# Kernel optimization log

Measured on AMD Instinct MI355X. Metric: run time of the kernel, lower is better.

## Reference

```python
import jax, jax.numpy as jnp
import numpy as np

# dims
N, E, H, ED, G = 50000, 1000000, 64, 16, 512
IN_C, OUT_C, L, T, OUT_N = 39, 128, 3, 2, 1
SLOPE = 0.01  # negative slope used by F.leaky_relu and GATConv(negative_slope=0.01)


def _seg_softmax(a, seg, n):
    # numerically-stable softmax over edges grouped by target segment
    m = jax.ops.segment_max(a, seg, num_segments=n)
    m = jnp.where(jnp.isfinite(m), m, 0.0)
    e = jnp.exp(a - m[seg])
    s = jax.ops.segment_sum(e, seg, num_segments=n)
    return e / (s[seg] + 1e-16)


def _gru(inp, h, wi, wh, bi, bh):
    # torch.nn.GRUCell: gates ordered (r, z, n)
    gi = inp @ wi.T + bi
    gh = h @ wh.T + bh
    ir, iz, i_n = jnp.split(gi, 3, axis=-1)
    hr, hz, h_n = jnp.split(gh, 3, axis=-1)
    r = jax.nn.sigmoid(ir + hr)
    z = jax.nn.sigmoid(iz + hz)
    n = jnp.tanh(i_n + r * h_n)
    return (1.0 - z) * n + z * h


def _forward(x, edge_attr,
             lin1_w, lin1_b,
             g_lin1_w, g_att_l, g_att_r, g_lin2_w, g_bias,
             gru0_wi, gru0_wh, gru0_bi, gru0_bh,
             conv_lin_w, conv_att_src, conv_att_dst, conv_bias,
             grul_wi, grul_wh, grul_bi, grul_bh,
             mol_lin_w, mol_att_src, mol_att_dst, mol_bias,
             mgru_wi, mgru_wh, mgru_bi, mgru_bh,
             lin2_w, lin2_b,
             src, dst, batch):
    x = jax.nn.leaky_relu(x @ lin1_w.T + lin1_b, SLOPE)  # [N,H]

    # ---- GATEConv ----
    xj, xi = x[src], x[dst]                               # [E,H]
    t = jax.nn.leaky_relu(jnp.concatenate([xj, edge_attr], -1) @ g_lin1_w.T, SLOPE)
    a = jax.nn.leaky_relu(t @ g_att_l + xi @ g_att_r, SLOPE)
    a = _seg_softmax(a, dst, N)
    h = jax.ops.segment_sum((xj @ g_lin2_w.T) * a[:, None], dst, num_segments=N) + g_bias
    h = jax.nn.elu(h)
    x = jax.nn.relu(_gru(h, x, gru0_wi, gru0_wh, gru0_bi, gru0_bh))

    # ---- GATConv atom layers ----
    for l in range(L - 1):
        hs = x @ conv_lin_w[l].T                          # [N,H]
        a = jax.nn.leaky_relu((hs @ conv_att_src[l])[src] + (hs @ conv_att_dst[l])[dst], SLOPE)
        a = _seg_softmax(a, dst, N)
        h = jax.ops.segment_sum(hs[src] * a[:, None], dst, num_segments=N) + conv_bias[l]
        h = jax.nn.elu(h)
        x = jax.nn.relu(_gru(h, x, grul_wi[l], grul_wh[l], grul_bi[l], grul_bh[l]))

    # ---- molecule-level attention readout ----
    out = jax.nn.relu(jax.ops.segment_sum(x, batch, num_segments=G))  # [G,H]
    for _ in range(T):
        hs = x @ mol_lin_w.T                              # [N,H]  (atoms = sources)
        hd = out @ mol_lin_w.T                            # [G,H]  (mols = targets)
        a = jax.nn.leaky_relu(hs @ mol_att_src + (hd @ mol_att_dst)[batch], SLOPE)
        a = _seg_softmax(a, batch, G)
        h = jax.ops.segment_sum(hs * a[:, None], batch, num_segments=G) + mol_bias
        h = jax.nn.elu(h)
        out = jax.nn.relu(_gru(h, out, mgru_wi, mgru_wh, mgru_bi, mgru_bh))

    out = out @ lin2_w.T + lin2_b                         # [G,OUT_C]
    return jnp.concatenate([out[None]] * OUT_N, axis=0)   # [OUT_N,G,OUT_C]


def setup_inputs() -> dict:
    key = jax.random.key(0)
    it = iter(jax.random.split(key, 48))

    def p(*shape):
        return jax.random.normal(next(it), shape, jnp.float32) * 0.1

    d = {}
    d["x"] = jax.random.normal(next(it), (N, IN_C), jnp.float32)
    d["edge_index"] = jax.random.randint(next(it), (2, E), 0, N, dtype=jnp.int32)
    d["edge_attr"] = jax.random.normal(next(it), (E, ED), jnp.float32)
    d["batch"] = jnp.sort(jax.random.randint(next(it), (N,), 0, G, dtype=jnp.int32))

    d["lin1_w"], d["lin1_b"] = p(H, IN_C), p(H)
    d["g_lin1_w"] = p(H, H + ED)
    d["g_att_l"], d["g_att_r"] = p(H), p(H)
    d["g_lin2_w"], d["g_bias"] = p(H, H), p(H)
    d["gru0_wi"], d["gru0_wh"] = p(3 * H, H), p(3 * H, H)
    d["gru0_bi"], d["gru0_bh"] = p(3 * H), p(3 * H)
    d["conv_lin_w"] = p(L - 1, H, H)
    d["conv_att_src"], d["conv_att_dst"] = p(L - 1, H), p(L - 1, H)
    d["conv_bias"] = p(L - 1, H)
    d["grul_wi"], d["grul_wh"] = p(L - 1, 3 * H, H), p(L - 1, 3 * H, H)
    d["grul_bi"], d["grul_bh"] = p(L - 1, 3 * H), p(L - 1, 3 * H)
    d["mol_lin_w"] = p(H, H)
    d["mol_att_src"], d["mol_att_dst"] = p(H), p(H)
    d["mol_bias"] = p(H)
    d["mgru_wi"], d["mgru_wh"] = p(3 * H, H), p(3 * H, H)
    d["mgru_bi"], d["mgru_bh"] = p(3 * H), p(3 * H)
    d["lin2_w"], d["lin2_b"] = p(OUT_C, H), p(OUT_C)
    return d


def reference(x, edge_index, edge_attr, batch,
              lin1_w, lin1_b,
              g_lin1_w, g_att_l, g_att_r, g_lin2_w, g_bias,
              gru0_wi, gru0_wh, gru0_bi, gru0_bh,
              conv_lin_w, conv_att_src, conv_att_dst, conv_bias,
              grul_wi, grul_wh, grul_bi, grul_bh,
              mol_lin_w, mol_att_src, mol_att_dst, mol_bias,
              mgru_wi, mgru_wh, mgru_bi, mgru_bh,
              lin2_w, lin2_b):
    src, dst = edge_index[0], edge_index[1]
    return _forward(x, edge_attr,
                    lin1_w, lin1_b,
                    g_lin1_w, g_att_l, g_att_r, g_lin2_w, g_bias,
                    gru0_wi, gru0_wh, gru0_bi, gru0_bh,
                    conv_lin_w, conv_att_src, conv_att_dst, conv_bias,
                    grul_wi, grul_wh, grul_bi, grul_bh,
                    mol_lin_w, mol_att_src, mol_att_dst, mol_bias,
                    mgru_wi, mgru_wh, mgru_bi, mgru_bh,
                    lin2_w, lin2_b,
                    src, dst, batch)
```

## Files before the change

kernel.cpp:

```cpp
#include <hip/hip_runtime.h>
#include <math.h>

#define N_NODES 50000
#define N_EDGES 1000000
#define NGRAPH  512
#define INC     39
#define SB 200
#define SC 250
#define NBKT 196
#define BIN_BLK 4096

typedef __attribute__((ext_vector_type(8))) short bf16x8;
typedef __attribute__((ext_vector_type(4))) float f32x4;
typedef __attribute__((ext_vector_type(4))) int i32x4;

__device__ __forceinline__ float lrelu(float x){ return fmaxf(0.01f*x, x); }
__device__ __forceinline__ float fexp(float x){ return __builtin_amdgcn_exp2f(x*1.4426950408889634f); }
__device__ __forceinline__ float frcp(float x){ return __builtin_amdgcn_rcpf(x); }
__device__ __forceinline__ float eluf (float x){ return x > 0.f ? x : fexp(x) - 1.f; }
__device__ __forceinline__ float sigm (float x){ return frcp(1.f + fexp(-x)); }
__device__ __forceinline__ float ftanh(float x){
  x = fminf(fmaxf(x, -15.f), 15.f);
  float e = __builtin_amdgcn_exp2f(x*2.8853900817779268f);
  return (e - 1.f)*frcp(e + 1.f);
}
__device__ __forceinline__ float rdlane(float v, int l){
  return __int_as_float(__builtin_amdgcn_readlane(__float_as_int(v), l));
}
__device__ __forceinline__ unsigned pk_bf16(float a, float b){
  unsigned r;
  asm volatile("v_cvt_pk_bf16_f32 %0, %1, %2" : "=v"(r) : "v"(a), "v"(b));
  return r;
}
__device__ __forceinline__ float bl(unsigned p){ return __uint_as_float(p << 16); }
__device__ __forceinline__ float bh(unsigned p){ return __uint_as_float(p & 0xffff0000u); }

__global__ __launch_bounds__(256) void k_hist(const int* __restrict__ dst,
                                              int* __restrict__ cnt) {
  int e = blockIdx.x*256 + threadIdx.x;
  if (e < N_EDGES) atomicAdd(&cnt[dst[e]], 1);
}

__global__ __launch_bounds__(256) void k_scanA(const int* __restrict__ cnt,
                                               int* __restrict__ bsum) {
  __shared__ int s[256];
  int t = threadIdx.x, b = blockIdx.x;
  int v = (t < SC) ? cnt[b*SC + t] : 0;
  s[t] = v; __syncthreads();
  for (int off = 128; off > 0; off >>= 1) {
    if (t < off) s[t] += s[t+off];
    __syncthreads();
  }
  if (t == 0) bsum[b] = s[0];
}

__global__ __launch_bounds__(256) void k_scanB(const int* __restrict__ bsum,
                                               int* __restrict__ boff,
                                               int* __restrict__ rowptrN) {
  __shared__ int s[256];
  int t = threadIdx.x;
  int v = (t < SB) ? bsum[t] : 0;
  s[t] = v; __syncthreads();
  for (int off = 1; off < 256; off <<= 1) {
    int x = (t >= off) ? s[t-off] : 0;
    __syncthreads();
    s[t] += x;
    __syncthreads();
  }
  if (t < SB) boff[t] = s[t] - v;
  if (t == 0) rowptrN[0] = N_EDGES;
}

__global__ __launch_bounds__(256) void k_scanC(const int* __restrict__ cnt,
                                               const int* __restrict__ boff,
                                               int* __restrict__ rowptr) {
  __shared__ int s[256];
  int t = threadIdx.x, b = blockIdx.x;
  int idx = b*SC + t;
  int v = (t < SC) ? cnt[idx] : 0;
  s[t] = v; __syncthreads();
  for (int off = 1; off < 256; off <<= 1) {
    int x = (t >= off) ? s[t-off] : 0;
    __syncthreads();
    s[t] += x;
    __syncthreads();
  }
  if (t < SC) rowptr[idx] = boff[b] + s[t] - v;
}

__global__ __launch_bounds__(256) void k_bstart(const int* __restrict__ rowptr,
                                                int* __restrict__ bstart,
                                                int* __restrict__ bcur) {
  int b = threadIdx.x;
  if (b <= NBKT) {
    int idx = b*256; if (idx > N_NODES) idx = N_NODES;
    int v = rowptr[idx];
    bstart[b] = v;
    if (b < NBKT) bcur[b] = v;
  }
}

__global__ __launch_bounds__(1024) void k_binA(const int* __restrict__ dst,
                                               const int* __restrict__ src,
                                               const float* __restrict__ p,
                                               int* __restrict__ bcur,
                                               int2* __restrict__ binned) {
  __shared__ int lcnt[NBKT];
  __shared__ int lbase[NBKT];
  __shared__ int gbase[NBKT];
  __shared__ int tmp[256];
  __shared__ int totsh;
  __shared__ int2 stage[BIN_BLK];
  const int t = threadIdx.x;
  const int e0 = blockIdx.x * BIN_BLK;
  for (int i = t; i < NBKT; i += 1024) lcnt[i] = 0;
  __syncthreads();
  int myb[4], myr[4], myd[4], mys[4]; float myp[4];
  #pragma unroll
  for (int u = 0; u < 4; ++u) {
    int e = e0 + u*1024 + t;
    if (e < N_EDGES) {
      int d = dst[e];
      myd[u] = d; mys[u] = src[e]; myp[u] = p[e];
      int b = d >> 8;
      myb[u] = b;
      myr[u] = atomicAdd(&lcnt[b], 1);
    } else myb[u] = -1;
  }
  __syncthreads();
  if (t < 256) tmp[t] = (t < NBKT) ? lcnt[t] : 0;
  __syncthreads();
  for (int off = 1; off < 256; off <<= 1) {
    int v = (t >= off && t < 256) ? tmp[t-off] : 0;
    __syncthreads();
    if (t < 256) tmp[t] += v;
    __syncthreads();
  }
  if (t < NBKT) lbase[t] = tmp[t] - lcnt[t];
  if (t == NBKT-1) totsh = tmp[t];
  if (t < NBKT && lcnt[t] > 0) gbase[t] = atomicAdd(&bcur[t], lcnt[t]);
  __syncthreads();
  #pragma unroll
  for (int u = 0; u < 4; ++u) {
    if (myb[u] >= 0) {
      int x = (mys[u] & 0xffff) | ((myd[u] & 255) << 16) | (myb[u] << 24);
      stage[lbase[myb[u]] + myr[u]] = make_int2(x, __float_as_int(myp[u]));
    }
  }
  __syncthreads();
  const int tot = totsh;
  for (int i = t; i < tot; i += 1024) {
    int2 r = stage[i];
    int b = (unsigned)r.x >> 24;
    binned[gbase[b] + (i - lbase[b])] = r;
  }
}

__global__ __launch_bounds__(1024) void k_binB(const int* __restrict__ rowptr,
                                               const int* __restrict__ bstart,
                                               const int2* __restrict__ binned,
                                               int2* __restrict__ sorted) {
  __shared__ int lcnt[256];
  const int b = blockIdx.x;
  const int base = bstart[b], end = bstart[b+1];
  const int t = threadIdx.x;
  if (t < 256) lcnt[t] = 0;
  __syncthreads();
  for (int i = base + t; i < end; i += 1024) {
    int2 r = binned[i];
    int dlow = (r.x >> 16) & 255;
    int rank = atomicAdd(&lcnt[dlow], 1);
    int pos = rowptr[b*256 + dlow] + rank;
    sorted[pos] = r;
  }
}

__global__ __launch_bounds__(512) void k_gbound(const int* __restrict__ batch,
                                                int* __restrict__ gstart) {
  int g = threadIdx.x;
  int lo = 0, hi = N_NODES;
  while (lo < hi) { int mid = (lo+hi)>>1; if (batch[mid] < g) lo = mid+1; else hi = mid; }
  gstart[g] = lo;
  if (g == 0) gstart[NGRAPH] = N_NODES;
}

__global__ __launch_bounds__(256) void k_wpack(const float* __restrict__ wi,
                                               const float* __restrict__ wh,
                                               unsigned short* __restrict__ o) {
  int i = blockIdx.x*256 + threadIdx.x;
  if (i < 192*64)      o[i]          = (unsigned short)(pk_bf16(wi[i], 0.f) & 0xffffu);
  else if (i < 2*192*64) o[i]        = (unsigned short)(pk_bf16(wh[i - 192*64], 0.f) & 0xffffu);
}

__global__ __launch_bounds__(256) void k_lin1(const float* __restrict__ x,
                                              const float* __restrict__ W,
                                              const float* __restrict__ b,
                                              float* __restrict__ out,
                                              const float* __restrict__ v1,
                                              float* __restrict__ o1) {
  __shared__ float wl[64*41];
  for (int idx = threadIdx.x; idx < 64*INC; idx += 256) {
    int r = idx / INC, c = idx - r*INC;
    wl[r*41+c] = W[idx];
  }
  __syncthreads();
  const int lane = threadIdx.x & 63;
  const int base = blockIdx.x*32 + (threadIdx.x>>6)*8;
  float h[8];
  #pragma unroll
  for (int i = 0; i < 8; ++i) {
    int n = base + i;
    h[i] = (n < N_NODES && lane < INC) ? x[n*INC + lane] : 0.f;
  }
  float acc[8] = {0,0,0,0,0,0,0,0};
  #pragma unroll
  for (int k = 0; k < INC; ++k) {
    float wv = wl[lane*41+k];
    #pragma unroll
    for (int i = 0; i < 8; ++i) acc[i] += rdlane(h[i], k) * wv;
  }
  float bb = b[lane];
  float attv = v1[lane];
  #pragma unroll
  for (int i = 0; i < 8; ++i) {
    int n = base + i;
    if (n >= N_NODES) continue;
    float val = lrelu(acc[i] + bb);
    out[n*64+lane] = val;
    float p = val * attv;
    #pragma unroll
    for (int s2 = 32; s2 > 0; s2 >>= 1) p += __shfl_xor(p, s2, 64);
    if (lane == 0) o1[n] = p;
  }
}

__global__ __launch_bounds__(256) void k_mmdual(const float* __restrict__ in,
                                                const float* __restrict__ W1,
                                                const float* __restrict__ W2,
                                                unsigned short* __restrict__ ubf,
                                                unsigned* __restrict__ ypk, int R) {
  __shared__ float wl[128*65];
  for (int idx = threadIdx.x; idx < 4096; idx += 256) {
    int r = idx >> 6, c = idx & 63;
    wl[r*65+c]      = W1[r*80 + c];
    wl[(64+r)*65+c] = W2[r*64 + c];
  }
  __syncthreads();
  const int lane = threadIdx.x & 63;
  const int base = blockIdx.x*32 + (threadIdx.x>>6)*8;
  float h[8];
  #pragma unroll
  for (int i = 0; i < 8; ++i) { int n = base+i; h[i] = (n < R) ? in[n*64+lane] : 0.f; }
  float accU[8] = {0,0,0,0,0,0,0,0};
  float accY[8] = {0,0,0,0,0,0,0,0};
  for (int k = 0; k < 64; ++k) {
    float wu = wl[lane*65+k], wy = wl[(64+lane)*65+k];
    #pragma unroll
    for (int i = 0; i < 8; ++i) {
      float hk = rdlane(h[i], k);
      accU[i] += hk*wu; accY[i] += hk*wy;
    }
  }
  #pragma unroll
  for (int i = 0; i < 8; ++i) {
    int n = base+i; if (n >= R) continue;
    ubf[n*64 + lane] = (unsigned short)(pk_bf16(accU[i], 0.f) & 0xffffu);
    float partner = __shfl_xor(accY[i], 1, 64);
    if (!(lane & 1)) ypk[n*32 + (lane>>1)] = pk_bf16(accY[i], partner);
  }
}

__global__ __launch_bounds__(256) void k_mm64(const float* __restrict__ in,
                                              const float* __restrict__ W, int rs,
                                              float* __restrict__ out,
                                              unsigned* __restrict__ outp, int R,
                                              const float* __restrict__ v1,
                                              const float* __restrict__ v2,
                                              float* __restrict__ o1,
                                              float* __restrict__ o2) {
  __shared__ float wl[64*65];
  for (int idx = threadIdx.x; idx < 4096; idx += 256) {
    int r = idx >> 6, c = idx & 63;
    wl[r*65+c] = W[r*rs + c];
  }
  __syncthreads();
  const int lane = threadIdx.x & 63;
  const int base = blockIdx.x*32 + (threadIdx.x>>6)*8;
  float h[8];
  #pragma unroll
  for (int i = 0; i < 8; ++i) { int n = base+i; h[i] = (n < R) ? in[n*64+lane] : 0.f; }
  float acc[8] = {0,0,0,0,0,0,0,0};
  for (int k = 0; k < 64; ++k) {
    float wv = wl[lane*65+k];
    #pragma unroll
    for (int i = 0; i < 8; ++i) acc[i] += rdlane(h[i], k) * wv;
  }
  float v1v = v1 ? v1[lane] : 0.f;
  float v2v = v2 ? v2[lane] : 0.f;
  #pragma unroll
  for (int i = 0; i < 8; ++i) {
    int n = base+i; if (n >= R) continue;
    if (out) out[n*64+lane] = acc[i];
    if (outp) {
      float partner = __shfl_xor(acc[i], 1, 64);
      if ((lane & 1) == 0) outp[n*32 + (lane>>1)] = pk_bf16(acc[i], partner);
    }
    if (o1) {
      float p1 = acc[i]*v1v;
      float p2 = acc[i]*v2v;
      #pragma unroll
      for (int s2 = 32; s2 > 0; s2 >>= 1) { p1 += __shfl_xor(p1, s2, 64); p2 += __shfl_xor(p2, s2, 64); }
      if (lane == 0) { o1[n] = p1; if (o2) o2[n] = p2; }
    }
  }
}

__global__ __launch_bounds__(256) void k_escore(const int* __restrict__ srcarr,
                                                const float* __restrict__ ea,
                                                const float* __restrict__ glin1,
                                                const float* __restrict__ attl,
                                                const unsigned short* __restrict__ ubf,
                                                float* __restrict__ pout) {
  const int lane = threadIdx.x & 63;
  const int l15 = lane & 15, lg = lane >> 4;
  const int gw = blockIdx.x*4 + (threadIdx.x >> 6);
  if (gw >= N_EDGES/64) return;
  float attlv[4];
  unsigned Bu[4][2];
  #pragma unroll
  for (int c = 0; c < 4; ++c) {
    const float4 b = *(const float4*)&glin1[(c*16 + l15)*80 + 64 + lg*4];
    Bu[c][0] = pk_bf16(b.x, b.y);
    Bu[c][1] = pk_bf16(b.z, b.w);
    attlv[c] = attl[c*16 + l15];
  }
  const int i0 = gw*64;
  i32x4 sv[4];
  #pragma unroll
  for (int it = 0; it < 4; ++it)
    sv[it] = *(const i32x4*)&srcarr[i0 + it*16 + 4*lg];
  f32x4 a[4];
  #pragma unroll
  for (int it = 0; it < 4; ++it)
    a[it] = __builtin_nontemporal_load((const f32x4*)&ea[(size_t)(i0 + it*16 + l15)*16 + lg*4]);
  unsigned short ug0[4][4], ug1[4][4];
  #pragma unroll
  for (int c = 0; c < 4; ++c)
    #pragma unroll
    for (int r = 0; r < 4; ++r)
      ug0[c][r] = ubf[(size_t)sv[0][r]*64 + c*16 + l15];
  #pragma unroll
  for (int it = 0; it < 4; ++it) {
    if (it + 1 < 4) {
      #pragma unroll
      for (int c = 0; c < 4; ++c)
        #pragma unroll
        for (int r = 0; r < 4; ++r)
          ug1[c][r] = ubf[(size_t)sv[it+1][r]*64 + c*16 + l15];
    }
    union { bf16x8 v; unsigned u[4]; } A;
    A.u[0] = pk_bf16(a[it][0], a[it][1]);
    A.u[1] = pk_bf16(a[it][2], a[it][3]);
    A.u[2] = 0; A.u[3] = 0;
    float p[4] = {0.f,0.f,0.f,0.f};
    #pragma unroll
    for (int c = 0; c < 4; ++c) {
      union { bf16x8 v; unsigned u[4]; } B;
      B.u[0] = Bu[c][0]; B.u[1] = Bu[c][1]; B.u[2] = 0; B.u[3] = 0;
      f32x4 z = {0.f,0.f,0.f,0.f};
      f32x4 acc = __builtin_amdgcn_mfma_f32_16x16x32_bf16(A.v, B.v, z, 0, 0, 0);
      #pragma unroll
      for (int r = 0; r < 4; ++r) {
        float t = lrelu(__uint_as_float(((unsigned)ug0[c][r]) << 16) + acc[r]);
        p[r] = fmaf(t, attlv[c], p[r]);
      }
    }
    #pragma unroll
    for (int r = 0; r < 4; ++r) {
      p[r] += __shfl_xor(p[r], 1, 64);
      p[r] += __shfl_xor(p[r], 2, 64);
      p[r] += __shfl_xor(p[r], 4, 64);
      p[r] += __shfl_xor(p[r], 8, 64);
    }
    if (l15 == 0) {
      f32x4 o = {p[0], p[1], p[2], p[3]};
      __builtin_nontemporal_store(o, (f32x4*)&pout[i0 + it*16 + 4*lg]);
    }
    #pragma unroll
    for (int c = 0; c < 4; ++c)
      #pragma unroll
      for (int r = 0; r < 4; ++r)
        ug0[c][r] = ug1[c][r];
  }
}

__global__ __launch_bounds__(256) void k_gate_agg(const int* __restrict__ rowptr,
                                                  const int2* __restrict__ sorted,
                                                  const float* __restrict__ xr,
                                                  const unsigned* __restrict__ ypk,
                                                  float* __restrict__ hagg) {
  __shared__ int   sS[4][64];
  __shared__ float sE[4][64];
  const int w = __builtin_amdgcn_readfirstlane(threadIdx.x >> 6);
  const int lane = threadIdx.x & 63;
  const int slot = lane >> 5, l2 = lane & 31;
  const int d = blockIdx.x*4 + w;
  const int r0 = __builtin_amdgcn_readfirstlane(rowptr[d]);
  const int r1 = __builtin_amdgcn_readfirstlane(rowptr[d+1]);
  const float xrd = xr[d];
  float accx = 0.f, accy = 0.f, ssum = 0.f;
  for (int base = r0; base < r1; base += 64) {
    int i = base + lane;
    int cnt = r1 - base; if (cnt > 64) cnt = 64;
    float ev = 0.f; int s = 0;
    if (i < r1) {
      int2 r = sorted[i];
      s = r.x & 0xffff;
      ev = fexp(lrelu(__int_as_float(r.y) + xrd));
    }
    sS[w][lane] = s; sE[w][lane] = ev;
    ssum += ev;
    for (int jb = 0; jb < cnt; jb += 16) {
      float e8[8]; unsigned p8[8];
      #pragma unroll
      for (int u = 0; u < 8; ++u) {
        int jj = jb + 2*u + slot;
        int svv; float evv;
        if (jj < cnt) { svv = sS[w][jj]; evv = sE[w][jj]; }
        else          { svv = 0; evv = 0.f; }
        e8[u] = evv;
        p8[u] = ypk[(size_t)svv*32 + l2];
      }
      #pragma unroll
      for (int u = 0; u < 8; ++u) {
        accx = fmaf(e8[u], bl(p8[u]), accx);
        accy = fmaf(e8[u], bh(p8[u]), accy);
      }
    }
  }
  #pragma unroll
  for (int sh = 32; sh > 0; sh >>= 1) ssum += __shfl_xor(ssum, sh, 64);
  accx += __shfl_xor(accx, 32, 64);
  accy += __shfl_xor(accy, 32, 64);
  float rs = frcp(ssum + 1e-16f);
  if (slot == 0) *(float2*)&hagg[d*64 + 2*l2] = make_float2(accx*rs, accy*rs);
}

__global__ __launch_bounds__(256) void k_conv_fused(const int* __restrict__ rowptr,
                                                    const int2* __restrict__ sorted,
                                                    const float* __restrict__ asn,
                                                    const float* __restrict__ adn,
                                                    const unsigned* __restrict__ hsb,
                                                    float* __restrict__ hagg) {
  __shared__ int   sS[4][64];
  __shared__ float sE[4][64];
  const int w = __builtin_amdgcn_readfirstlane(threadIdx.x >> 6);
  const int lane = threadIdx.x & 63;
  const int slot = lane >> 5, l2 = lane & 31;
  const int d = blockIdx.x*4 + w;
  const int r0 = __builtin_amdgcn_readfirstlane(rowptr[d]);
  const int r1 = __builtin_amdgcn_readfirstlane(rowptr[d+1]);
  float adnd = adn[d];
  float accx = 0.f, accy = 0.f, ssum = 0.f;
  for (int base = r0; base < r1; base += 64) {
    int i = base + lane;
    int cnt = r1 - base; if (cnt > 64) cnt = 64;
    float ev = 0.f; int s = 0;
    if (i < r1) { s = sorted[i].x & 0xffff; ev = fexp(lrelu(asn[s] + adnd)); }
    sS[w][lane] = s; sE[w][lane] = ev;
    ssum += ev;
    for (int jb = 0; jb < cnt; jb += 16) {
      float e8[8]; unsigned p8[8];
      #pragma unroll
      for (int u = 0; u < 8; ++u) {
        int jj = jb + 2*u + slot;
        int svv; float evv;
        if (jj < cnt) { svv = sS[w][jj]; evv = sE[w][jj]; }
        else          { svv = 0; evv = 0.f; }
        e8[u] = evv;
        p8[u] = hsb[(size_t)svv*32 + l2];
      }
      #pragma unroll
      for (int u = 0; u < 8; ++u) {
        accx = fmaf(e8[u], bl(p8[u]), accx);
        accy = fmaf(e8[u], bh(p8[u]), accy);
      }
    }
  }
  #pragma unroll
  for (int sh = 32; sh > 0; sh >>= 1) ssum += __shfl_xor(ssum, sh, 64);
  accx += __shfl_xor(accx, 32, 64);
  accy += __shfl_xor(accy, 32, 64);
  float rs = frcp(ssum + 1e-16f);
  if (slot == 0) *(float2*)&hagg[d*64 + 2*l2] = make_float2(accx*rs, accy*rs);
}

__global__ __launch_bounds__(256) void k_gruM(const float* __restrict__ inp,
                                              const float* __restrict__ pbias,
                                              const float* __restrict__ hid,
                                              const unsigned short* __restrict__ wibf,
                                              const unsigned short* __restrict__ whbf,
                                              const float* __restrict__ bi,
                                              const float* __restrict__ bh2,
                                              float* __restrict__ out, int R) {
  const int lane = threadIdx.x & 63;
  const int l15 = lane & 15, lg = lane >> 4;
  const int n0 = blockIdx.x*64 + (threadIdx.x >> 6)*16;
  if (n0 >= R) return;
  union BF { bf16x8 v; unsigned u[4]; };
  BF Ai[2], Ah[2];
  const int arow = n0 + l15;
  const bool av = arow < R;
  const float* ibase = inp + (size_t)arow*64;
  const float* hbase = hid + (size_t)arow*64;
  #pragma unroll
  for (int c = 0; c < 2; ++c) {
    const int k0 = c*32 + lg*8;
    float4 p0 = *(const float4*)&pbias[k0];
    float4 p1 = *(const float4*)&pbias[k0+4];
    float4 v0, v1, h0, h1;
    if (av) {
      v0 = *(const float4*)&ibase[k0];   v1 = *(const float4*)&ibase[k0+4];
      h0 = *(const float4*)&hbase[k0];   h1 = *(const float4*)&hbase[k0+4];
    } else {
      v0 = v1 = h0 = h1 = make_float4(0.f,0.f,0.f,0.f);
      p0 = p1 = make_float4(0.f,0.f,0.f,0.f);
    }
    Ai[c].u[0] = pk_bf16(eluf(v0.x+p0.x), eluf(v0.y+p0.y));
    Ai[c].u[1] = pk_bf16(eluf(v0.z+p0.z), eluf(v0.w+p0.w));
    Ai[c].u[2] = pk_bf16(eluf(v1.x+p1.x), eluf(v1.y+p1.y));
    Ai[c].u[3] = pk_bf16(eluf(v1.z+p1.z), eluf(v1.w+p1.w));
    Ah[c].u[0] = pk_bf16(h0.x, h0.y);
    Ah[c].u[1] = pk_bf16(h0.z, h0.w);
    Ah[c].u[2] = pk_bf16(h1.x, h1.y);
    Ah[c].u[3] = pk_bf16(h1.z, h1.w);
  }
  f32x4 rz[8], ni[4], nh[4];
  #pragma unroll
  for (int t = 0; t < 8; ++t) rz[t] = (f32x4){0.f,0.f,0.f,0.f};
  #pragma unroll
  for (int t = 0; t < 4; ++t) { ni[t] = (f32x4){0.f,0.f,0.f,0.f}; nh[t] = (f32x4){0.f,0.f,0.f,0.f}; }
  #pragma unroll
  for (int t = 0; t < 12; ++t) {
    BF Bi0, Bi1, Bh0, Bh1;
    const size_t off = ((size_t)(t*16 + l15))*64 + lg*8;
    Bi0.v = *(const bf16x8*)&wibf[off];
    Bi1.v = *(const bf16x8*)&wibf[off + 32];
    Bh0.v = *(const bf16x8*)&whbf[off];
    Bh1.v = *(const bf16x8*)&whbf[off + 32];
    if (t < 8) {
      f32x4 a = rz[t];
      a = __builtin_amdgcn_mfma_f32_16x16x32_bf16(Ai[0].v, Bi0.v, a, 0, 0, 0);
      a = __builtin_amdgcn_mfma_f32_16x16x32_bf16(Ai[1].v, Bi1.v, a, 0, 0, 0);
      a = __builtin_amdgcn_mfma_f32_16x16x32_bf16(Ah[0].v, Bh0.v, a, 0, 0, 0);
      a = __builtin_amdgcn_mfma_f32_16x16x32_bf16(Ah[1].v, Bh1.v, a, 0, 0, 0);
      rz[t] = a;
    } else {
      f32x4 a = ni[t-8];
      a = __builtin_amdgcn_mfma_f32_16x16x32_bf16(Ai[0].v, Bi0.v, a, 0, 0, 0);
      a = __builtin_amdgcn_mfma_f32_16x16x32_bf16(Ai[1].v, Bi1.v, a, 0, 0, 0);
      ni[t-8] = a;
      f32x4 b = nh[t-8];
      b = __builtin_amdgcn_mfma_f32_16x16x32_bf16(Ah[0].v, Bh0.v, b, 0, 0, 0);
      b = __builtin_amdgcn_mfma_f32_16x16x32_bf16(Ah[1].v, Bh1.v, b, 0, 0, 0);
      nh[t-8] = b;
    }
  }
  float bsum[8], binv[4], bhnv[4];
  #pragma unroll
  for (int t = 0; t < 8; ++t) bsum[t] = bi[t*16+l15] + bh2[t*16+l15];
  #pragma unroll
  for (int t = 0; t < 4; ++t) {
    binv[t] = bi[128 + t*16 + l15];
    bhnv[t] = bh2[128 + t*16 + l15];
  }
  #pragma unroll
  for (int reg = 0; reg < 4; ++reg) {
    const int node = n0 + 4*lg + reg;
    if (node >= R) continue;
    #pragma unroll
    for (int tt = 0; tt < 4; ++tt) {
      float r  = sigm(rz[tt][reg] + bsum[tt]);
      float z  = sigm(rz[4+tt][reg] + bsum[4+tt]);
      float nn = ftanh(ni[tt][reg] + binv[tt] + r*(nh[tt][reg] + bhnv[tt]));
      float hh = hid[(size_t)node*64 + tt*16 + l15];
      float o  = (1.f - z)*nn + z*hh;
      out[(size_t)node*64 + tt*16 + l15] = fmaxf(o, 0.f);
    }
  }
}

__global__ __launch_bounds__(256) void k_molsum_p(const int* __restrict__ gstart,
                                                  const float* __restrict__ x,
                                                  float* __restrict__ part) {
  int idx = blockIdx.x*4 + (threadIdx.x>>6);
  if (idx >= NGRAPH*8) return;
  int g = idx >> 3, sl = idx & 7;
  int lane = threadIdx.x & 63;
  int n0 = gstart[g], n1 = gstart[g+1];
  int len = n1 - n0;
  int b0 = n0 + (len*sl >> 3), b1 = n0 + (len*(sl+1) >> 3);
  float acc = 0.f;
  for (int n = b0; n < b1; ++n) acc += x[n*64+lane];
  part[idx*64+lane] = acc;
}

__global__ __launch_bounds__(256) void k_molsum_c(const float* __restrict__ part,
                                                  float* __restrict__ outg) {
  int g = blockIdx.x*4 + (threadIdx.x>>6);
  if (g >= NGRAPH) return;
  int lane = threadIdx.x & 63;
  float a = 0.f;
  #pragma unroll
  for (int s = 0; s < 8; ++s) a += part[(g*8+s)*64+lane];
  outg[g*64+lane] = fmaxf(a, 0.f);
}

__global__ __launch_bounds__(256) void k_molhd(const float* __restrict__ outg,
                                               const float* __restrict__ W,
                                               const float* __restrict__ attd,
                                               float* __restrict__ addg) {
  __shared__ float wl[64*65];
  for (int idx = threadIdx.x; idx < 4096; idx += 256) wl[(idx>>6)*65+(idx&63)] = W[idx];
  __syncthreads();
  int g = blockIdx.x*4 + (threadIdx.x>>6);
  if (g >= NGRAPH) return;
  int lane = threadIdx.x & 63;
  float og = outg[g*64+lane];
  float hd = 0.f;
  #pragma unroll
  for (int k = 0; k < 64; ++k) hd += rdlane(og, k) * wl[lane*65+k];
  float p = hd * attd[lane];
  #pragma unroll
  for (int sh = 32; sh > 0; sh >>= 1) p += __shfl_xor(p, sh, 64);
  if (lane == 0) addg[g] = p;
}

__global__ __launch_bounds__(256) void k_molp(const int* __restrict__ gstart,
                                              const float* __restrict__ addg,
                                              const float* __restrict__ asn,
                                              const float* __restrict__ y,
                                              float* __restrict__ part_acc,
                                              float* __restrict__ part_ss) {
  int idx = blockIdx.x*4 + (threadIdx.x>>6);
  if (idx >= NGRAPH*8) return;
  int g = idx >> 3, sl = idx & 7;
  int lane = threadIdx.x & 63;
  int n0 = gstart[g], n1 = gstart[g+1];
  int len = n1 - n0;
  int b0 = n0 + (len*sl >> 3), b1 = n0 + (len*(sl+1) >> 3);
  float adg = addg[g];
  float acc = 0.f, ss = 0.f;
  for (int n = b0; n < b1; ++n) {
    float ev = fexp(lrelu(asn[n] + adg));
    acc += ev * y[n*64+lane];
    ss  += ev;
  }
  part_acc[idx*64+lane] = acc;
  if (lane == 0) part_ss[idx] = ss;
}

__global__ __launch_bounds__(256) void k_molc(const float* __restrict__ part_acc,
                                              const float* __restrict__ part_ss,
                                              float* __restrict__ hg) {
  int g = blockIdx.x*4 + (threadIdx.x>>6);
  if (g >= NGRAPH) return;
  int lane = threadIdx.x & 63;
  float a = 0.f, ss = 0.f;
  #pragma unroll
  for (int s = 0; s < 8; ++s) {
    a  += part_acc[(g*8+s)*64+lane];
    ss += part_ss[g*8+s];
  }
  hg[g*64+lane] = a * frcp(ss + 1e-16f);
}

__global__ __launch_bounds__(128) void k_final(const float* __restrict__ outg,
                                               const float* __restrict__ W,
                                               const float* __restrict__ b,
                                               float* __restrict__ out) {
  __shared__ float og[64];
  int g = blockIdx.x;
  if (threadIdx.x < 64) og[threadIdx.x] = outg[g*64+threadIdx.x];
  __syncthreads();
  int o = threadIdx.x;
  float acc = b[o];
  for (int k = 0; k < 64; ++k) acc += og[k]*W[o*64+k];
  out[g*128+o] = acc;
}

extern "C" void kernel_launch(void* const* d_in, const int* in_sizes, int n_in,
                              void* d_out, int out_size, void* d_ws, size_t ws_size,
                              hipStream_t stream) {
  const float* x_in     = (const float*)d_in[0];
  const int*   eidx     = (const int*)  d_in[1];
  const float* eattr    = (const float*)d_in[2];
  const int*   batch    = (const int*)  d_in[3];
  const float* lin1_w   = (const float*)d_in[4];
  const float* lin1_b   = (const float*)d_in[5];
  const float* g_lin1_w = (const float*)d_in[6];
  const float* g_att_l  = (const float*)d_in[7];
  const float* g_att_r  = (const float*)d_in[8];
  const float* g_lin2_w = (const float*)d_in[9];
  const float* g_bias   = (const float*)d_in[10];
  const float* gru0_wi  = (const float*)d_in[11];
  const float* gru0_wh  = (const float*)d_in[12];
  const float* gru0_bi  = (const float*)d_in[13];
  const float* gru0_bh  = (const float*)d_in[14];
  const float* conv_lin_w   = (const float*)d_in[15];
  const float* conv_att_src = (const float*)d_in[16];
  const float* conv_att_dst = (const float*)d_in[17];
  const float* conv_bias    = (const float*)d_in[18];
  const float* grul_wi  = (const float*)d_in[19];
  const float* grul_wh  = (const float*)d_in[20];
  const float* grul_bi  = (const float*)d_in[21];
  const float* grul_bh  = (const float*)d_in[22];
  const float* mol_lin_w    = (const float*)d_in[23];
  const float* mol_att_src  = (const float*)d_in[24];
  const float* mol_att_dst  = (const float*)d_in[25];
  const float* mol_bias     = (const float*)d_in[26];
  const float* mgru_wi  = (const float*)d_in[27];
  const float* mgru_wh  = (const float*)d_in[28];
  const float* mgru_bi  = (const float*)d_in[29];
  const float* mgru_bh  = (const float*)d_in[30];
  const float* lin2_w   = (const float*)d_in[31];
  const float* lin2_b   = (const float*)d_in[32];

  const int N64 = N_NODES*64;
  float* ws     = (float*)d_ws;
  float* xA     = ws;
  float* xB     = xA + N64;
  float* uy     = xB + N64;
  float* hagg   = uy + 2*N64;
  float* sc1    = hagg + N64;
  float* sc2    = sc1 + N_NODES;
  float* pbuf   = sc2 + N_NODES;
  float* outg   = pbuf + N_EDGES;
  int* icnt   = (int*)(outg + NGRAPH*64);
  int* rowptr = icnt + N_NODES;
  int2* binned = (int2*)(rowptr + N_NODES + 2);
  int2* sorted = binned + N_EDGES;
  int* gstart = (int*)(sorted + N_EDGES);
  int* bsum   = gstart + NGRAPH+1;
  int* boff   = bsum + SB;
  int* bstart = boff + SB;
  int* bcur   = bstart + NBKT+1;
  unsigned short* wpk = (unsigned short*)(bcur + NBKT + 4);

  unsigned short* ubf = (unsigned short*)uy;
  unsigned* ypk = (unsigned*)(uy + N64);
  unsigned* hsb = (unsigned*)uy;

  float* part_acc = (float*)binned;
  float* part_ss  = part_acc + NGRAPH*8*64;
  float* addg     = part_ss + NGRAPH*8;

  const int* src = eidx;
  const int* dst = eidx + N_EDGES;

  const int nbN32 = (N_NODES + 31)/32;
  const int nbN4  = (N_NODES + 3)/4;
  const int nbN64 = (N_NODES + 63)/64;
  const int nbE   = (N_EDGES + 255)/256;
  const int nbG4  = (NGRAPH + 3)/4;
  const int nbG8  = (NGRAPH*8 + 3)/4;
  const int nbES  = (N_EDGES/64 + 3)/4;
  const int PAIR  = 2*192*64;

  hipMemsetAsync(icnt, 0, N_NODES*sizeof(int), stream);
  k_hist<<<nbE, 256, 0, stream>>>(dst, icnt);
  k_scanA<<<SB, 256, 0, stream>>>(icnt, bsum);
  k_scanB<<<1, 256, 0, stream>>>(bsum, boff, rowptr + N_NODES);
  k_scanC<<<SB, 256, 0, stream>>>(icnt, boff, rowptr);
  k_bstart<<<1, 256, 0, stream>>>(rowptr, bstart, bcur);
  k_gbound<<<1, 512, 0, stream>>>(batch, gstart);

  k_wpack<<<(PAIR+255)/256, 256, 0, stream>>>(gru0_wi, gru0_wh, wpk);
  k_wpack<<<(PAIR+255)/256, 256, 0, stream>>>(grul_wi, grul_wh, wpk + PAIR);
  k_wpack<<<(PAIR+255)/256, 256, 0, stream>>>(grul_wi + 192*64, grul_wh + 192*64, wpk + 2*PAIR);
  k_wpack<<<(PAIR+255)/256, 256, 0, stream>>>(mgru_wi, mgru_wh, wpk + 3*PAIR);

  k_lin1<<<nbN32, 256, 0, stream>>>(x_in, lin1_w, lin1_b, xA, g_att_r, sc1);

  k_mmdual<<<nbN32, 256, 0, stream>>>(xA, g_lin1_w, g_lin2_w, ubf, ypk, N_NODES);
  k_escore<<<nbES, 256, 0, stream>>>(src, eattr, g_lin1_w, g_att_l, ubf, pbuf);
  k_binA<<<(N_EDGES + BIN_BLK-1)/BIN_BLK, 1024, 0, stream>>>(dst, src, pbuf, bcur, binned);
  k_binB<<<NBKT, 1024, 0, stream>>>(rowptr, bstart, binned, sorted);
  k_gate_agg<<<nbN4, 256, 0, stream>>>(rowptr, sorted, sc1, ypk, hagg);
  k_gruM<<<nbN64, 256, 0, stream>>>(hagg, g_bias, xA, wpk, wpk + 192*64,
                                    gru0_bi, gru0_bh, xB, N_NODES);

  float* xcur = xB; float* xoth = xA;

  for (int l = 0; l < 2; ++l) {
    k_mm64<<<nbN32, 256, 0, stream>>>(xcur, conv_lin_w + l*64*64, 64, nullptr, hsb, N_NODES,
                                      conv_att_src + l*64, conv_att_dst + l*64, sc1, sc2);
    k_conv_fused<<<nbN4, 256, 0, stream>>>(rowptr, sorted, sc1, sc2, hsb, hagg);
    k_gruM<<<nbN64, 256, 0, stream>>>(hagg, conv_bias + l*64, xcur,
                                      wpk + (1+l)*PAIR, wpk + (1+l)*PAIR + 192*64,
                                      grul_bi + l*192, grul_bh + l*192, xoth, N_NODES);
    float* t = xcur; xcur = xoth; xoth = t;
  }

  float* ymol = uy;
  k_molsum_p<<<nbG8, 256, 0, stream>>>(gstart, xcur, part_acc);
  k_molsum_c<<<nbG4, 256, 0, stream>>>(part_acc, outg);
  k_mm64<<<nbN32, 256, 0, stream>>>(xcur, mol_lin_w, 64, ymol, nullptr, N_NODES,
                                    mol_att_src, nullptr, sc1, nullptr);
  for (int t = 0; t < 2; ++t) {
    k_molhd<<<nbG4, 256, 0, stream>>>(outg, mol_lin_w, mol_att_dst, addg);
    k_molp<<<nbG8, 256, 0, stream>>>(gstart, addg, sc1, ymol, part_acc, part_ss);
    k_molc<<<nbG4, 256, 0, stream>>>(part_acc, part_ss, hagg);
    k_gruM<<<(NGRAPH+63)/64, 256, 0, stream>>>(hagg, mol_bias, outg,
                                               wpk + 3*PAIR, wpk + 3*PAIR + 192*64,
                                               mgru_bi, mgru_bh, outg, NGRAPH);
  }

  k_final<<<NGRAPH, 128, 0, stream>>>(outg, lin2_w, lin2_b, (float*)d_out);
}
```

Before: 496.1 us.

## Build CSR via bucket histogram with in-bin scan; MFMA lin1 with split bf16

Replaces the per-node histogram and the three-pass scan with a coarse per-bucket histogram (shared-memory atomics) and a single small scan. Each bucket's per-node row pointers are now computed inside binB through a local histogram and scan, which removes several launches and the global per-node atomics. lin1 is rewritten to use bf16 MFMA, with the input split into hi and lo bf16 parts to keep precision. The cost is an extra pass over binned data in binB, and weights rounded to bf16 in lin1.

```diff
diff --git a/kernel.cpp b/kernel.cpp
--- a/kernel.cpp
+++ b/kernel.cpp
@@ -5,8 +5,6 @@
 #define N_EDGES 1000000
 #define NGRAPH  512
 #define INC     39
-#define SB 200
-#define SC 250
 #define NBKT 196
 #define BIN_BLK 4096
 
@@ -34,32 +32,30 @@
 }
 __device__ __forceinline__ float bl(unsigned p){ return __uint_as_float(p << 16); }
 __device__ __forceinline__ float bh(unsigned p){ return __uint_as_float(p & 0xffff0000u); }
-
-__global__ __launch_bounds__(256) void k_hist(const int* __restrict__ dst,
-                                              int* __restrict__ cnt) {
-  int e = blockIdx.x*256 + threadIdx.x;
-  if (e < N_EDGES) atomicAdd(&cnt[dst[e]], 1);
-}
-
-__global__ __launch_bounds__(256) void k_scanA(const int* __restrict__ cnt,
-                                               int* __restrict__ bsum) {
-  __shared__ int s[256];
-  int t = threadIdx.x, b = blockIdx.x;
-  int v = (t < SC) ? cnt[b*SC + t] : 0;
-  s[t] = v; __syncthreads();
-  for (int off = 128; off > 0; off >>= 1) {
-    if (t < off) s[t] += s[t+off];
-    __syncthreads();
-  }
-  if (t == 0) bsum[b] = s[0];
-}
-
-__global__ __launch_bounds__(256) void k_scanB(const int* __restrict__ bsum,
-                                               int* __restrict__ boff,
+__device__ __forceinline__ float tobf16f(float v){ return __uint_as_float(pk_bf16(v, 0.f) << 16); }
+
+__global__ __launch_bounds__(256) void k_bhist(const int* __restrict__ dst,
+                                               int* __restrict__ bcnt) {
+  __shared__ int h[NBKT];
+  for (int i = threadIdx.x; i < NBKT; i += 256) h[i] = 0;
+  __syncthreads();
+  const int e0 = blockIdx.x * BIN_BLK;
+  #pragma unroll 4
+  for (int u = 0; u < 16; ++u) {
+    int e = e0 + u*256 + threadIdx.x;
+    if (e < N_EDGES) atomicAdd(&h[dst[e] >> 8], 1);
+  }
+  __syncthreads();
+  for (int i = threadIdx.x; i < NBKT; i += 256) if (h[i]) atomicAdd(&bcnt[i], h[i]);
+}
+
+__global__ __launch_bounds__(256) void k_bscan(const int* __restrict__ bcnt,
+                                               int* __restrict__ bstart,
+                                               int* __restrict__ bcur,
                                                int* __restrict__ rowptrN) {
   __shared__ int s[256];
   int t = threadIdx.x;
-  int v = (t < SB) ? bsum[t] : 0;
+  int v = (t < NBKT) ? bcnt[t] : 0;
   s[t] = v; __syncthreads();
   for (int off = 1; off < 256; off <<= 1) {
     int x = (t >= off) ? s[t-off] : 0;
@@ -67,37 +63,8 @@
     s[t] += x;
     __syncthreads();
   }
-  if (t < SB) boff[t] = s[t] - v;
-  if (t == 0) rowptrN[0] = N_EDGES;
-}
-
-__global__ __launch_bounds__(256) void k_scanC(const int* __restrict__ cnt,
-                                               const int* __restrict__ boff,
-                                               int* __restrict__ rowptr) {
-  __shared__ int s[256];
-  int t = threadIdx.x, b = blockIdx.x;
-  int idx = b*SC + t;
-  int v = (t < SC) ? cnt[idx] : 0;
-  s[t] = v; __syncthreads();
-  for (int off = 1; off < 256; off <<= 1) {
-    int x = (t >= off) ? s[t-off] : 0;
-    __syncthreads();
-    s[t] += x;
-    __syncthreads();
-  }
-  if (t < SC) rowptr[idx] = boff[b] + s[t] - v;
-}
-
-__global__ __launch_bounds__(256) void k_bstart(const int* __restrict__ rowptr,
-                                                int* __restrict__ bstart,
-                                                int* __restrict__ bcur) {
-  int b = threadIdx.x;
-  if (b <= NBKT) {
-    int idx = b*256; if (idx > N_NODES) idx = N_NODES;
-    int v = rowptr[idx];
-    bstart[b] = v;
-    if (b < NBKT) bcur[b] = v;
-  }
+  if (t < NBKT) { int st = s[t] - v; bstart[t] = st; bcur[t] = st; }
+  if (t == 0) { bstart[NBKT] = N_EDGES; rowptrN[0] = N_EDGES; }
 }
 
 __global__ __launch_bounds__(1024) void k_binA(const int* __restrict__ dst,
@@ -156,22 +123,41 @@
   }
 }
 
-__global__ __launch_bounds__(1024) void k_binB(const int* __restrict__ rowptr,
-                                               const int* __restrict__ bstart,
+__global__ __launch_bounds__(1024) void k_binB(const int* __restrict__ bstart,
                                                const int2* __restrict__ binned,
-                                               int2* __restrict__ sorted) {
+                                               int2* __restrict__ sorted,
+                                               int* __restrict__ rowptr) {
   __shared__ int lcnt[256];
+  __shared__ int loc[256];
   const int b = blockIdx.x;
   const int base = bstart[b], end = bstart[b+1];
   const int t = threadIdx.x;
   if (t < 256) lcnt[t] = 0;
   __syncthreads();
+  for (int i = base + t; i < end; i += 1024)
+    atomicAdd(&lcnt[(binned[i].x >> 16) & 255], 1);
+  __syncthreads();
+  if (t < 256) loc[t] = lcnt[t];
+  __syncthreads();
+  for (int off = 1; off < 256; off <<= 1) {
+    int v = (t >= off && t < 256) ? loc[t-off] : 0;
+    __syncthreads();
+    if (t < 256) loc[t] += v;
+    __syncthreads();
+  }
+  if (t < 256) {
+    int st = base + loc[t] - lcnt[t];
+    loc[t] = st;
+    int node = b*256 + t;
+    if (node < N_NODES) rowptr[node] = st;
+    lcnt[t] = 0;
+  }
+  __syncthreads();
   for (int i = base + t; i < end; i += 1024) {
     int2 r = binned[i];
     int dlow = (r.x >> 16) & 255;
     int rank = atomicAdd(&lcnt[dlow], 1);
-    int pos = rowptr[b*256 + dlow] + rank;
-    sorted[pos] = r;
+    sorted[loc[dlow] + rank] = r;
   }
 }
 
@@ -192,45 +178,84 @@
   else if (i < 2*192*64) o[i]        = (unsigned short)(pk_bf16(wh[i - 192*64], 0.f) & 0xffffu);
 }
 
-__global__ __launch_bounds__(256) void k_lin1(const float* __restrict__ x,
-                                              const float* __restrict__ W,
-                                              const float* __restrict__ b,
-                                              float* __restrict__ out,
-                                              const float* __restrict__ v1,
-                                              float* __restrict__ o1) {
-  __shared__ float wl[64*41];
-  for (int idx = threadIdx.x; idx < 64*INC; idx += 256) {
-    int r = idx / INC, c = idx - r*INC;
-    wl[r*41+c] = W[idx];
-  }
-  __syncthreads();
+__global__ __launch_bounds__(256) void k_lin1M(const float* __restrict__ x,
+                                               const float* __restrict__ W,
+                                               const float* __restrict__ b,
+                                               const float* __restrict__ v1,
+                                               float* __restrict__ out,
+                                               float* __restrict__ o1) {
   const int lane = threadIdx.x & 63;
-  const int base = blockIdx.x*32 + (threadIdx.x>>6)*8;
-  float h[8];
-  #pragma unroll
-  for (int i = 0; i < 8; ++i) {
-    int n = base + i;
-    h[i] = (n < N_NODES && lane < INC) ? x[n*INC + lane] : 0.f;
-  }
-  float acc[8] = {0,0,0,0,0,0,0,0};
-  #pragma unroll
-  for (int k = 0; k < INC; ++k) {
-    float wv = wl[lane*41+k];
-    #pragma unroll
-    for (int i = 0; i < 8; ++i) acc[i] += rdlane(h[i], k) * wv;
-  }
-  float bb = b[lane];
-  float attv = v1[lane];
-  #pragma unroll
-  for (int i = 0; i < 8; ++i) {
-    int n = base + i;
-    if (n >= N_NODES) continue;
-    float val = lrelu(acc[i] + bb);
-    out[n*64+lane] = val;
-    float p = val * attv;
-    #pragma unroll
-    for (int s2 = 32; s2 > 0; s2 >>= 1) p += __shfl_xor(p, s2, 64);
-    if (lane == 0) o1[n] = p;
+  const int l15 = lane & 15, lg = lane >> 4;
+  const int n0 = blockIdx.x*64 + (threadIdx.x >> 6)*16;
+  if (n0 >= N_NODES) return;
+  union BF { bf16x8 v; unsigned u[4]; };
+  BF Bf[3][4];
+  #pragma unroll
+  for (int c = 0; c < 3; ++c) {
+    int kv0 = c*32 + lg*8;
+    int off = (kv0 < 48) ? kv0 : (kv0 - 48);
+    int cnt = 39 - off; cnt = cnt < 0 ? 0 : (cnt > 8 ? 8 : cnt);
+    #pragma unroll
+    for (int ct = 0; ct < 4; ++ct) {
+      const float* wrow = W + (ct*16 + l15)*INC;
+      float w8[8];
+      #pragma unroll
+      for (int j = 0; j < 8; ++j) w8[j] = (j < cnt) ? wrow[off+j] : 0.f;
+      Bf[c][ct].u[0] = pk_bf16(w8[0], w8[1]);
+      Bf[c][ct].u[1] = pk_bf16(w8[2], w8[3]);
+      Bf[c][ct].u[2] = pk_bf16(w8[4], w8[5]);
+      Bf[c][ct].u[3] = pk_bf16(w8[6], w8[7]);
+    }
+  }
+  const int arow = n0 + l15;
+  const bool av = arow < N_NODES;
+  const float* xrow = x + (size_t)arow*INC;
+  BF A[3];
+  #pragma unroll
+  for (int c = 0; c < 3; ++c) {
+    int kv0 = c*32 + lg*8;
+    int islo = (kv0 >= 48);
+    int off = islo ? (kv0 - 48) : kv0;
+    int cnt = 39 - off; cnt = cnt < 0 ? 0 : (cnt > 8 ? 8 : cnt);
+    float a8[8];
+    #pragma unroll
+    for (int j = 0; j < 8; ++j) {
+      float v = (av && j < cnt) ? xrow[off+j] : 0.f;
+      if (islo) v = v - tobf16f(v);
+      a8[j] = v;
+    }
+    A[c].u[0] = pk_bf16(a8[0], a8[1]);
+    A[c].u[1] = pk_bf16(a8[2], a8[3]);
+    A[c].u[2] = pk_bf16(a8[4], a8[5]);
+    A[c].u[3] = pk_bf16(a8[6], a8[7]);
+  }
+  f32x4 acc[4];
+  #pragma unroll
+  for (int ct = 0; ct < 4; ++ct) acc[ct] = (f32x4){0.f,0.f,0.f,0.f};
+  #pragma unroll
+  for (int c = 0; c < 3; ++c)
+    #pragma unroll
+    for (int ct = 0; ct < 4; ++ct)
+      acc[ct] = __builtin_amdgcn_mfma_f32_16x16x32_bf16(A[c].v, Bf[c][ct].v, acc[ct], 0, 0, 0);
+  float bb[4], attv[4];
+  #pragma unroll
+  for (int ct = 0; ct < 4; ++ct) { bb[ct] = b[ct*16+l15]; attv[ct] = v1[ct*16+l15]; }
+  #pragma unroll
+  for (int reg = 0; reg < 4; ++reg) {
+    const int node = n0 + 4*lg + reg;
+    const bool nv = node < N_NODES;
+    float pr = 0.f;
+    #pragma unroll
+    for (int ct = 0; ct < 4; ++ct) {
+      float val = lrelu(acc[ct][reg] + bb[ct]);
+      if (nv) out[(size_t)node*64 + ct*16 + l15] = val;
+      pr = fmaf(val, attv[ct], pr);
+    }
+    pr += __shfl_xor(pr, 1, 64);
+    pr += __shfl_xor(pr, 2, 64);
+    pr += __shfl_xor(pr, 4, 64);
+    pr += __shfl_xor(pr, 8, 64);
+    if (l15 == 0 && nv) o1[node] = pr;
   }
 }
 
@@ -736,14 +761,12 @@
   float* sc2    = sc1 + N_NODES;
   float* pbuf   = sc2 + N_NODES;
   float* outg   = pbuf + N_EDGES;
-  int* icnt   = (int*)(outg + NGRAPH*64);
-  int* rowptr = icnt + N_NODES;
+  int* bcnt   = (int*)(outg + NGRAPH*64);
+  int* rowptr = bcnt + N_NODES;
   int2* binned = (int2*)(rowptr + N_NODES + 2);
   int2* sorted = binned + N_EDGES;
   int* gstart = (int*)(sorted + N_EDGES);
-  int* bsum   = gstart + NGRAPH+1;
-  int* boff   = bsum + SB;
-  int* bstart = boff + SB;
+  int* bstart = gstart + NGRAPH+1;
   int* bcur   = bstart + NBKT+1;
   unsigned short* wpk = (unsigned short*)(bcur + NBKT + 4);
 
@@ -761,18 +784,15 @@
   const int nbN32 = (N_NODES + 31)/32;
   const int nbN4  = (N_NODES + 3)/4;
   const int nbN64 = (N_NODES + 63)/64;
-  const int nbE   = (N_EDGES + 255)/256;
   const int nbG4  = (NGRAPH + 3)/4;
   const int nbG8  = (NGRAPH*8 + 3)/4;
   const int nbES  = (N_EDGES/64 + 3)/4;
+  const int nbBIN = (N_EDGES + BIN_BLK-1)/BIN_BLK;
   const int PAIR  = 2*192*64;
 
-  hipMemsetAsync(icnt, 0, N_NODES*sizeof(int), stream);
-  k_hist<<<nbE, 256, 0, stream>>>(dst, icnt);
-  k_scanA<<<SB, 256, 0, stream>>>(icnt, bsum);
-  k_scanB<<<1, 256, 0, stream>>>(bsum, boff, rowptr + N_NODES);
-  k_scanC<<<SB, 256, 0, stream>>>(icnt, boff, rowptr);
-  k_bstart<<<1, 256, 0, stream>>>(rowptr, bstart, bcur);
+  hipMemsetAsync(bcnt, 0, NBKT*sizeof(int), stream);
+  k_bhist<<<nbBIN, 256, 0, stream>>>(dst, bcnt);
+  k_bscan<<<1, 256, 0, stream>>>(bcnt, bstart, bcur, rowptr + N_NODES);
   k_gbound<<<1, 512, 0, stream>>>(batch, gstart);
 
   k_wpack<<<(PAIR+255)/256, 256, 0, stream>>>(gru0_wi, gru0_wh, wpk);
@@ -780,12 +800,12 @@
   k_wpack<<<(PAIR+255)/256, 256, 0, stream>>>(grul_wi + 192*64, grul_wh + 192*64, wpk + 2*PAIR);
   k_wpack<<<(PAIR+255)/256, 256, 0, stream>>>(mgru_wi, mgru_wh, wpk + 3*PAIR);
 
-  k_lin1<<<nbN32, 256, 0, stream>>>(x_in, lin1_w, lin1_b, xA, g_att_r, sc1);
+  k_lin1M<<<nbN64, 256, 0, stream>>>(x_in, lin1_w, lin1_b, g_att_r, xA, sc1);
 
   k_mmdual<<<nbN32, 256, 0, stream>>>(xA, g_lin1_w, g_lin2_w, ubf, ypk, N_NODES);
   k_escore<<<nbES, 256, 0, stream>>>(src, eattr, g_lin1_w, g_att_l, ubf, pbuf);
-  k_binA<<<(N_EDGES + BIN_BLK-1)/BIN_BLK, 1024, 0, stream>>>(dst, src, pbuf, bcur, binned);
-  k_binB<<<NBKT, 1024, 0, stream>>>(rowptr, bstart, binned, sorted);
+  k_binA<<<nbBIN, 1024, 0, stream>>>(dst, src, pbuf, bcur, binned);
+  k_binB<<<NBKT, 1024, 0, stream>>>(bstart, binned, sorted, rowptr);
   k_gate_agg<<<nbN4, 256, 0, stream>>>(rowptr, sorted, sc1, ypk, hagg);
   k_gruM<<<nbN64, 256, 0, stream>>>(hagg, g_bias, xA, wpk, wpk + 192*64,
                                     gru0_bi, gru0_bh, xB, N_NODES);
```

Result: faster. 454.7 us (-8.3%).
